# Performance work log

Hardware: AMD Instinct MI355X
Metric: run time of the kernel (lower is better)

The kernel has to match this reference:

```python
import jax, jax.numpy as jnp
import numpy as np

N_BONDS = 50000
N_EDGES = 600000
BOND_DIM = 64
SPH_DIM = 64
UNITS = 64


def setup_inputs() -> dict:
    key = jax.random.key(0)
    k1, k2, k3, k4, k5 = jax.random.split(key, 5)
    bond_features = jax.random.normal(k1, (N_BONDS, BOND_DIM), dtype=jnp.float32)
    edges_sph_features = jax.random.normal(k2, (N_EDGES, SPH_DIM), dtype=jnp.float32)
    # column 0: sorted segment ids (tf.math.segment_sum requires sorted ids)
    seg = jnp.sort(jax.random.randint(k3, (N_EDGES,), 0, N_BONDS, dtype=jnp.int32))
    nbr = jax.random.randint(k4, (N_EDGES,), 0, N_BONDS, dtype=jnp.int32)
    edges_neighbor = jnp.stack([seg, nbr], axis=1)  # [n_edges, 2]
    kernel = jax.random.normal(k5, (BOND_DIM + SPH_DIM, UNITS), dtype=jnp.float32) * 0.05
    bias = jnp.zeros((UNITS,), dtype=jnp.float32)
    return {
        "bond_features": bond_features,
        "edges_sph_features": edges_sph_features,
        "edges_neighbor": edges_neighbor,
        "kernel": kernel,
        "bias": bias,
    }


def reference(bond_features, edges_sph_features, edges_neighbor, kernel, bias):
    # gather bond features of the neighboring bond for each edge (line-graph)
    gathered = bond_features[edges_neighbor[:, 1]]            # [E, bond_dim]
    concated = jnp.concatenate([gathered, edges_sph_features], axis=-1)  # [E, bond_dim+sph_dim]
    # scatter-reduce into segments (sorted ids; fixed num_segments for jit)
    aggregated = jax.ops.segment_sum(
        concated, edges_neighbor[:, 0], num_segments=N_BONDS,
        indices_are_sorted=True,
    )  # [n_bonds, bond_dim+sph_dim]
    return aggregated @ kernel + bias
```

## Files before the change

### kernel.cpp

```cpp
#include <hip/hip_runtime.h>

#define N_BONDS 50000
#define N_EDGES 600000
#define R_BONDS 4
#define THREADS 512
#define BONDS_PER_BLOCK 32

typedef float f4 __attribute__((ext_vector_type(4)));

__device__ __forceinline__ float bcastf(float v, int l) {
    return __builtin_bit_cast(float, __builtin_amdgcn_readlane(__builtin_bit_cast(int, v), l));
}
__device__ __forceinline__ f4 f4zero() { return (f4){0.f, 0.f, 0.f, 0.f}; }
__device__ __forceinline__ void fma4(f4& a, float s, const f4& b) {
    a.x = fmaf(s, b.x, a.x); a.y = fmaf(s, b.y, a.y);
    a.z = fmaf(s, b.z, a.z); a.w = fmaf(s, b.w, a.w);
}

__global__ __launch_bounds__(256)
void fill_starts(const int* __restrict__ edges, int* __restrict__ starts) {
    const int e = blockIdx.x * blockDim.x + threadIdx.x;
    if (e >= N_EDGES) return;
    const int2* edges2 = (const int2*)edges;
    const int s  = edges2[e].x;
    const int sp = (e == 0) ? -1 : edges2[e - 1].x;
    for (int b = sp + 1; b <= s; ++b) starts[b] = e;
    if (e == N_EDGES - 1)
        for (int b = s + 1; b <= N_BONDS; ++b) starts[b] = N_EDGES;
}

__global__ __launch_bounds__(THREADS, 4)
void fused_gather_segsum_mm(const float* __restrict__ bond,
                            const float* __restrict__ sph,
                            const int*   __restrict__ edges,
                            const float* __restrict__ Kmat,
                            const float* __restrict__ bias,
                            const int*   __restrict__ starts,
                            float* __restrict__ out)
{
    __shared__ float ldsK[128 * 64];
    const int tid  = threadIdx.x;
    const int lane = tid & 63;
    const int wid  = tid >> 6;
    const int fl   = lane & 15;
    const int sg   = lane >> 4;

    {
        const f4* K4 = (const f4*)Kmat;
        f4*       L4 = (f4*)ldsK;
        #pragma unroll
        for (int i = 0; i < 4; ++i) L4[tid + i * THREADS] = K4[tid + i * THREADS];
    }
    __syncthreads();

    const int b0 = blockIdx.x * BONDS_PER_BLOCK + wid * R_BONDS;
    if (b0 >= N_BONDS) return;

    int st[R_BONDS + 1];
    #pragma unroll
    for (int r = 0; r <= R_BONDS; ++r)
        st[r] = __builtin_amdgcn_readfirstlane(starts[b0 + r]);

    const int eb    = st[0];
    const int total = st[R_BONDS] - eb;

    const f4*   bond4  = (const f4*)bond;
    const f4*   sph4   = (const f4*)sph;
    const int2* edges2 = (const int2*)edges;

    float slotG[R_BONDS], slotS[R_BONDS];
    f4 aG = f4zero(), aS = f4zero();
    int r = 0, cs = 0, bnd = st[1] - eb;

    auto txr = [&](f4 v) -> float {
        v.x += __shfl_xor(v.x, 16); v.y += __shfl_xor(v.y, 16);
        v.z += __shfl_xor(v.z, 16); v.w += __shfl_xor(v.w, 16);
        v.x += __shfl_xor(v.x, 32); v.y += __shfl_xor(v.y, 32);
        v.z += __shfl_xor(v.z, 32); v.w += __shfl_xor(v.w, 32);
        const int src = lane >> 2;
        const float s0 = __shfl(v.x, src), s1 = __shfl(v.y, src);
        const float s2 = __shfl(v.z, src), s3 = __shfl(v.w, src);
        const float r01 = (lane & 1) ? s1 : s0;
        const float r23 = (lane & 1) ? s3 : s2;
        return (lane & 2) ? r23 : r01;
    };

    auto slowpath = [&](int q, f4 GV, f4 SV) {
        const int qe = q + sg;
        while (true) {
            const float m = (qe >= cs && qe < bnd) ? 1.f : 0.f;
            fma4(aG, m, GV); fma4(aS, m, SV);
            if (bnd > q + 4) break;
            const float tG = txr(aG), tS = txr(aS);
            #pragma unroll
            for (int rr = 0; rr < R_BONDS; ++rr)
                if (rr == r) { slotG[rr] = tG; slotS[rr] = tS; }
            aG = f4zero(); aS = f4zero();
            cs = bnd;
            ++r;
            if (r >= R_BONDS) { bnd = 0x7fffffff; break; }
            #pragma unroll
            for (int rr = 2; rr <= R_BONDS; ++rr)
                if (r + 1 == rr) bnd = st[rr] - eb;
        }
    };

    int w0 = 0;
    while (w0 < total) {
        int wlen = total - w0; if (wlen > 64) wlen = 64;
        int2 p = make_int2(0, 0);
        if (lane < wlen) p = edges2[eb + w0 + lane];
        const int ng = (wlen + 3) >> 2;

        f4 gA, sA, gB, sB, gC, sC, gD, sD;

#define ISS(QQ, GV, SV) do { \
        if ((QQ) < ng) { \
            const int idx_ = (QQ) * 4 + sg; \
            const int nbr_ = __shfl(p.y, idx_); \
            int qe_ = w0 + idx_; if (qe_ >= total) qe_ = total - 1; \
            GV = bond4[nbr_ * 16 + fl]; \
            SV = __builtin_nontemporal_load(&sph4[(eb + qe_) * 16 + fl]); \
        } else { GV = f4zero(); SV = f4zero(); } } while (0)

#define ACC(QQ, GV, SV) do { \
        const int q_ = w0 + (QQ) * 4; \
        if (q_ + 4 <= bnd) { aG += GV; aS += SV; } \
        else slowpath(q_, GV, SV); } while (0)

        ISS(0, gA, sA); ISS(1, gB, sB); ISS(2, gC, sC); ISS(3, gD, sD);
        int q = 0;
        for (; q + 4 <= ng; q += 4) {
            ACC(q + 0, gA, sA); ISS(q + 4, gA, sA);
            ACC(q + 1, gB, sB); ISS(q + 5, gB, sB);
            ACC(q + 2, gC, sC); ISS(q + 6, gC, sC);
            ACC(q + 3, gD, sD); ISS(q + 7, gD, sD);
        }
        if (q + 0 < ng) ACC(q + 0, gA, sA);
        if (q + 1 < ng) ACC(q + 1, gB, sB);
        if (q + 2 < ng) ACC(q + 2, gC, sC);
#undef ISS
#undef ACC
        w0 += wlen;
    }

    {
        const float tG = txr(aG), tS = txr(aS);
        #pragma unroll
        for (int rr = 0; rr < R_BONDS; ++rr) {
            if (rr == r)     { slotG[rr] = tG;  slotS[rr] = tS; }
            else if (rr > r) { slotG[rr] = 0.f; slotS[rr] = 0.f; }
        }
    }

    float acc[R_BONDS];
    const float bl = bias[lane];
    #pragma unroll
    for (int rr = 0; rr < R_BONDS; ++rr) acc[rr] = bl;

    #pragma unroll 4
    for (int d = 0; d < 64; ++d) {
        const float kt = ldsK[d * 64 + lane];
        const float kb = ldsK[(64 + d) * 64 + lane];
        #pragma unroll
        for (int rr = 0; rr < R_BONDS; ++rr) {
            acc[rr] = fmaf(bcastf(slotG[rr], d), kt, acc[rr]);
            acc[rr] = fmaf(bcastf(slotS[rr], d), kb, acc[rr]);
        }
    }

    #pragma unroll
    for (int rr = 0; rr < R_BONDS; ++rr)
        if (b0 + rr < N_BONDS)
            __builtin_nontemporal_store(acc[rr], &out[(b0 + rr) * 64 + lane]);
}

extern "C" void kernel_launch(void* const* d_in, const int* in_sizes, int n_in,
                              void* d_out, int out_size, void* d_ws, size_t ws_size,
                              hipStream_t stream) {
    const float* bond  = (const float*)d_in[0];
    const float* sph   = (const float*)d_in[1];
    const int*   edges = (const int*)d_in[2];
    const float* Kmat  = (const float*)d_in[3];
    const float* bias  = (const float*)d_in[4];
    float* out  = (float*)d_out;
    int* starts = (int*)d_ws;

    fill_starts<<<(N_EDGES + 255) / 256, 256, 0, stream>>>(edges, starts);

    const int nblocks = (N_BONDS + BONDS_PER_BLOCK - 1) / BONDS_PER_BLOCK;
    fused_gather_segsum_mm<<<nblocks, THREADS, 0, stream>>>(bond, sph, edges, Kmat,
                                                            bias, starts, out);
}
```

Baseline: 76.43 us.

## Premultiply bond features by kernel before gather and split into three kernels

Uses linearity to multiply bond_features by the top half of the kernel once per bond, before the gather. The gather/segment-sum kernel then writes the reduced gathered part straight to out and the sph sum to a workspace buffer, and a final kernel applies the bottom half of the kernel plus bias. This removes the in-kernel matmul and the large LDS tile from the memory-bound gather loop, and it also moves to 8 bonds per wave with 256 threads. In exchange it adds two launches and extra round trips of 50000x64 intermediates through global memory. A fused fallback is kept for when the workspace is too small.

```diff
diff --git a/kernel.cpp b/kernel.cpp
--- a/kernel.cpp
+++ b/kernel.cpp
@@ -2,8 +2,8 @@
 
 #define N_BONDS 50000
 #define N_EDGES 600000
-#define R_BONDS 4
-#define THREADS 512
+#define R_BONDS 8
+#define THREADS 256
 #define BONDS_PER_BLOCK 32
 
 typedef float f4 __attribute__((ext_vector_type(4)));
@@ -29,49 +29,227 @@
         for (int b = s + 1; b <= N_BONDS; ++b) starts[b] = N_EDGES;
 }
 
+__global__ __launch_bounds__(256, 4)
+void premul_bond(const float* __restrict__ bond, const float* __restrict__ Kmat,
+                 float* __restrict__ bondK) {
+    __shared__ float ldsK[64 * 64];
+    const int tid = threadIdx.x, lane = tid & 63, wid = tid >> 6;
+    {
+        const f4* K4 = (const f4*)Kmat;
+        f4* L4 = (f4*)ldsK;
+        #pragma unroll
+        for (int i = 0; i < 4; ++i) L4[tid + i * 256] = K4[tid + i * 256];
+    }
+    __syncthreads();
+    const int row0 = blockIdx.x * BONDS_PER_BLOCK + wid * R_BONDS;
+    if (row0 >= N_BONDS) return;
+
+    float rowv[R_BONDS];
+    #pragma unroll
+    for (int r = 0; r < R_BONDS; ++r) {
+        int ri = row0 + r; if (ri >= N_BONDS) ri = N_BONDS - 1;
+        rowv[r] = __builtin_nontemporal_load(&bond[ri * 64 + lane]);
+    }
+    float acc[R_BONDS];
+    #pragma unroll
+    for (int r = 0; r < R_BONDS; ++r) acc[r] = 0.f;
+
+    #pragma unroll 4
+    for (int d = 0; d < 64; ++d) {
+        const float k = ldsK[d * 64 + lane];
+        #pragma unroll
+        for (int r = 0; r < R_BONDS; ++r)
+            acc[r] = fmaf(bcastf(rowv[r], d), k, acc[r]);
+    }
+    #pragma unroll
+    for (int r = 0; r < R_BONDS; ++r)
+        if (row0 + r < N_BONDS)
+            __builtin_nontemporal_store(acc[r], &bondK[(row0 + r) * 64 + lane]);
+}
+
 __global__ __launch_bounds__(THREADS, 4)
-void fused_gather_segsum_mm(const float* __restrict__ bond,
-                            const float* __restrict__ sph,
-                            const int*   __restrict__ edges,
-                            const float* __restrict__ Kmat,
-                            const float* __restrict__ bias,
-                            const int*   __restrict__ starts,
-                            float* __restrict__ out)
-{
-    __shared__ float ldsK[128 * 64];
-    const int tid  = threadIdx.x;
+void gather_segsum(const float* __restrict__ bondK, const float* __restrict__ sph,
+                   const int* __restrict__ edges, const int* __restrict__ starts,
+                   float* __restrict__ outG, float* __restrict__ Sbuf) {
+    const int tid = threadIdx.x;
     const int lane = tid & 63;
     const int wid  = tid >> 6;
     const int fl   = lane & 15;
     const int sg   = lane >> 4;
 
-    {
-        const f4* K4 = (const f4*)Kmat;
-        f4*       L4 = (f4*)ldsK;
-        #pragma unroll
-        for (int i = 0; i < 4; ++i) L4[tid + i * THREADS] = K4[tid + i * THREADS];
-    }
-    __syncthreads();
-
     const int b0 = blockIdx.x * BONDS_PER_BLOCK + wid * R_BONDS;
     if (b0 >= N_BONDS) return;
 
     int st[R_BONDS + 1];
     #pragma unroll
-    for (int r = 0; r <= R_BONDS; ++r)
-        st[r] = __builtin_amdgcn_readfirstlane(starts[b0 + r]);
-
-    const int eb    = st[0];
-    const int total = st[R_BONDS] - eb;
-
-    const f4*   bond4  = (const f4*)bond;
-    const f4*   sph4   = (const f4*)sph;
+    for (int r = 0; r <= R_BONDS; ++r) {
+        int ix = b0 + r; if (ix > N_BONDS) ix = N_BONDS;
+        st[r] = __builtin_amdgcn_readfirstlane(starts[ix]);
+    }
+    const int eb = st[0], total = st[R_BONDS] - eb;
+
+    const f4*   g4 = (const f4*)bondK;
+    const f4*   s4 = (const f4*)sph;
     const int2* edges2 = (const int2*)edges;
-
+    f4* oG = (f4*)outG;
+    f4* oS = (f4*)Sbuf;
+    const bool storer = (sg == 0);
+
+    f4 aG = f4zero(), aS = f4zero();
+    int r = 0, cs = 0, bnd = st[1] - eb;
+
+    auto xr = [&](f4 v) -> f4 {
+        v.x += __shfl_xor(v.x, 16); v.y += __shfl_xor(v.y, 16);
+        v.z += __shfl_xor(v.z, 16); v.w += __shfl_xor(v.w, 16);
+        v.x += __shfl_xor(v.x, 32); v.y += __shfl_xor(v.y, 32);
+        v.z += __shfl_xor(v.z, 32); v.w += __shfl_xor(v.w, 32);
+        return v;
+    };
+
+    auto slowpath = [&](int q, f4 GV, f4 SV) {
+        const int qe = q + sg;
+        while (true) {
+            const float m = (qe >= cs && qe < bnd) ? 1.f : 0.f;
+            fma4(aG, m, GV); fma4(aS, m, SV);
+            if (bnd > q + 4) break;
+            const f4 cg = xr(aG), csv = xr(aS);
+            if (storer && b0 + r < N_BONDS) {
+                __builtin_nontemporal_store(cg,  &oG[(b0 + r) * 16 + fl]);
+                __builtin_nontemporal_store(csv, &oS[(b0 + r) * 16 + fl]);
+            }
+            aG = f4zero(); aS = f4zero();
+            cs = bnd;
+            ++r;
+            if (r >= R_BONDS) { bnd = 0x7fffffff; break; }
+            #pragma unroll
+            for (int rr = 2; rr <= R_BONDS; ++rr)
+                if (r + 1 == rr) bnd = st[rr] - eb;
+        }
+    };
+
+    int w0 = 0;
+    while (w0 < total) {
+        int wlen = total - w0; if (wlen > 64) wlen = 64;
+        int2 p = make_int2(0, 0);
+        if (lane < wlen) p = edges2[eb + w0 + lane];
+        const int ng = (wlen + 3) >> 2;
+
+        f4 gA, sA, gB, sB, gC, sC, gD, sD;
+
+#define ISS(QQ, GV, SV) do { \
+        if ((QQ) < ng) { \
+            const int idx_ = (QQ) * 4 + sg; \
+            const int nbr_ = __shfl(p.y, idx_); \
+            int qe_ = w0 + idx_; if (qe_ >= total) qe_ = total - 1; \
+            GV = g4[nbr_ * 16 + fl]; \
+            SV = __builtin_nontemporal_load(&s4[(eb + qe_) * 16 + fl]); \
+        } else { GV = f4zero(); SV = f4zero(); } } while (0)
+
+#define ACC(QQ, GV, SV) do { \
+        const int q_ = w0 + (QQ) * 4; \
+        if (q_ + 4 <= bnd) { aG += GV; aS += SV; } \
+        else slowpath(q_, GV, SV); } while (0)
+
+        ISS(0, gA, sA); ISS(1, gB, sB); ISS(2, gC, sC); ISS(3, gD, sD);
+        int q = 0;
+        for (; q + 4 <= ng; q += 4) {
+            ACC(q + 0, gA, sA); ISS(q + 4, gA, sA);
+            ACC(q + 1, gB, sB); ISS(q + 5, gB, sB);
+            ACC(q + 2, gC, sC); ISS(q + 6, gC, sC);
+            ACC(q + 3, gD, sD); ISS(q + 7, gD, sD);
+        }
+        if (q + 0 < ng) ACC(q + 0, gA, sA);
+        if (q + 1 < ng) ACC(q + 1, gB, sB);
+        if (q + 2 < ng) ACC(q + 2, gC, sC);
+#undef ISS
+#undef ACC
+        w0 += wlen;
+    }
+
+    {
+        const f4 cg = xr(aG), csv = xr(aS);
+        if (r < R_BONDS && storer && b0 + r < N_BONDS) {
+            __builtin_nontemporal_store(cg,  &oG[(b0 + r) * 16 + fl]);
+            __builtin_nontemporal_store(csv, &oS[(b0 + r) * 16 + fl]);
+        }
+        const f4 z = f4zero();
+        for (int bb = r + 1; bb < R_BONDS; ++bb) {
+            if (storer && b0 + bb < N_BONDS) {
+                __builtin_nontemporal_store(z, &oG[(b0 + bb) * 16 + fl]);
+                __builtin_nontemporal_store(z, &oS[(b0 + bb) * 16 + fl]);
+            }
+        }
+    }
+}
+
+__global__ __launch_bounds__(256, 4)
+void finish_mm(const float* __restrict__ Sbuf, const float* __restrict__ Kmat,
+               const float* __restrict__ bias, float* __restrict__ out) {
+    __shared__ float ldsK[64 * 64];
+    const int tid = threadIdx.x, lane = tid & 63, wid = tid >> 6;
+    {
+        const f4* K4 = (const f4*)Kmat;
+        f4* L4 = (f4*)ldsK;
+        #pragma unroll
+        for (int i = 0; i < 4; ++i) L4[tid + i * 256] = K4[1024 + tid + i * 256];
+    }
+    __syncthreads();
+    const int row0 = blockIdx.x * BONDS_PER_BLOCK + wid * R_BONDS;
+    if (row0 >= N_BONDS) return;
+
+    const float bl = bias[lane];
+    float rowv[R_BONDS], acc[R_BONDS];
+    #pragma unroll
+    for (int r = 0; r < R_BONDS; ++r) {
+        int ri = row0 + r; if (ri >= N_BONDS) ri = N_BONDS - 1;
+        rowv[r] = __builtin_nontemporal_load(&Sbuf[ri * 64 + lane]);
+        acc[r]  = out[ri * 64 + lane] + bl;
+    }
+    #pragma unroll 4
+    for (int d = 0; d < 64; ++d) {
+        const float k = ldsK[d * 64 + lane];
+        #pragma unroll
+        for (int r = 0; r < R_BONDS; ++r)
+            acc[r] = fmaf(bcastf(rowv[r], d), k, acc[r]);
+    }
+    #pragma unroll
+    for (int r = 0; r < R_BONDS; ++r)
+        if (row0 + r < N_BONDS)
+            __builtin_nontemporal_store(acc[r], &out[(row0 + r) * 64 + lane]);
+}
+
+__global__ __launch_bounds__(THREADS, 4)
+void fused_fallback(const float* __restrict__ bond, const float* __restrict__ sph,
+                    const int* __restrict__ edges, const float* __restrict__ Kmat,
+                    const float* __restrict__ bias, const int* __restrict__ starts,
+                    float* __restrict__ out) {
+    __shared__ float ldsK[128 * 64];
+    const int tid = threadIdx.x, lane = tid & 63, wid = tid >> 6;
+    const int fl = lane & 15, sg = lane >> 4;
+    const float bl = bias[lane];
+    const int b0 = blockIdx.x * BONDS_PER_BLOCK + wid * R_BONDS;
+    int stv[R_BONDS + 1];
+    #pragma unroll
+    for (int r = 0; r <= R_BONDS; ++r) {
+        int ix = b0 + r; if (ix > N_BONDS) ix = N_BONDS;
+        stv[r] = starts[ix];
+    }
+    {
+        const f4* K4 = (const f4*)Kmat; f4* L4 = (f4*)ldsK;
+        #pragma unroll
+        for (int i = 0; i < 8; ++i) L4[tid + i * THREADS] = K4[tid + i * THREADS];
+    }
+    __syncthreads();
+    if (b0 >= N_BONDS) return;
+    int st[R_BONDS + 1];
+    #pragma unroll
+    for (int r = 0; r <= R_BONDS; ++r) st[r] = __builtin_amdgcn_readfirstlane(stv[r]);
+    const int eb = st[0], total = st[R_BONDS] - eb;
+    const f4* bond4 = (const f4*)bond; const f4* sph4 = (const f4*)sph;
+    const int2* edges2 = (const int2*)edges;
     float slotG[R_BONDS], slotS[R_BONDS];
     f4 aG = f4zero(), aS = f4zero();
     int r = 0, cs = 0, bnd = st[1] - eb;
-
     auto txr = [&](f4 v) -> float {
         v.x += __shfl_xor(v.x, 16); v.y += __shfl_xor(v.y, 16);
         v.z += __shfl_xor(v.z, 16); v.w += __shfl_xor(v.w, 16);
@@ -84,7 +262,6 @@
         const float r23 = (lane & 1) ? s3 : s2;
         return (lane & 2) ? r23 : r01;
     };
-
     auto slowpath = [&](int q, f4 GV, f4 SV) {
         const int qe = q + sg;
         while (true) {
@@ -96,24 +273,20 @@
             for (int rr = 0; rr < R_BONDS; ++rr)
                 if (rr == r) { slotG[rr] = tG; slotS[rr] = tS; }
             aG = f4zero(); aS = f4zero();
-            cs = bnd;
-            ++r;
+            cs = bnd; ++r;
             if (r >= R_BONDS) { bnd = 0x7fffffff; break; }
             #pragma unroll
             for (int rr = 2; rr <= R_BONDS; ++rr)
                 if (r + 1 == rr) bnd = st[rr] - eb;
         }
     };
-
     int w0 = 0;
     while (w0 < total) {
         int wlen = total - w0; if (wlen > 64) wlen = 64;
         int2 p = make_int2(0, 0);
         if (lane < wlen) p = edges2[eb + w0 + lane];
         const int ng = (wlen + 3) >> 2;
-
         f4 gA, sA, gB, sB, gC, sC, gD, sD;
-
 #define ISS(QQ, GV, SV) do { \
         if ((QQ) < ng) { \
             const int idx_ = (QQ) * 4 + sg; \
@@ -122,12 +295,10 @@
             GV = bond4[nbr_ * 16 + fl]; \
             SV = __builtin_nontemporal_load(&sph4[(eb + qe_) * 16 + fl]); \
         } else { GV = f4zero(); SV = f4zero(); } } while (0)
-
 #define ACC(QQ, GV, SV) do { \
         const int q_ = w0 + (QQ) * 4; \
         if (q_ + 4 <= bnd) { aG += GV; aS += SV; } \
         else slowpath(q_, GV, SV); } while (0)
-
         ISS(0, gA, sA); ISS(1, gB, sB); ISS(2, gC, sC); ISS(3, gD, sD);
         int q = 0;
         for (; q + 4 <= ng; q += 4) {
@@ -143,7 +314,6 @@
 #undef ACC
         w0 += wlen;
     }
-
     {
         const float tG = txr(aG), tS = txr(aS);
         #pragma unroll
@@ -152,12 +322,9 @@
             else if (rr > r) { slotG[rr] = 0.f; slotS[rr] = 0.f; }
         }
     }
-
     float acc[R_BONDS];
-    const float bl = bias[lane];
     #pragma unroll
     for (int rr = 0; rr < R_BONDS; ++rr) acc[rr] = bl;
-
     #pragma unroll 4
     for (int d = 0; d < 64; ++d) {
         const float kt = ldsK[d * 64 + lane];
@@ -168,7 +335,6 @@
             acc[rr] = fmaf(bcastf(slotS[rr], d), kb, acc[rr]);
         }
     }
-
     #pragma unroll
     for (int rr = 0; rr < R_BONDS; ++rr)
         if (b0 + rr < N_BONDS)
@@ -183,12 +349,24 @@
     const int*   edges = (const int*)d_in[2];
     const float* Kmat  = (const float*)d_in[3];
     const float* bias  = (const float*)d_in[4];
-    float* out  = (float*)d_out;
-    int* starts = (int*)d_ws;
+    float* out = (float*)d_out;
+
+    int*   starts = (int*)d_ws;
+    float* bondK  = (float*)((char*)d_ws + 262144);
+    float* Sbuf   = (float*)((char*)d_ws + 262144 + (size_t)N_BONDS * 64 * 4);
+
+    const size_t need = 262144 + 2ull * N_BONDS * 64 * 4;
+    const int nblocks = (N_BONDS + BONDS_PER_BLOCK - 1) / BONDS_PER_BLOCK;
 
     fill_starts<<<(N_EDGES + 255) / 256, 256, 0, stream>>>(edges, starts);
 
-    const int nblocks = (N_BONDS + BONDS_PER_BLOCK - 1) / BONDS_PER_BLOCK;
-    fused_gather_segsum_mm<<<nblocks, THREADS, 0, stream>>>(bond, sph, edges, Kmat,
-                                                            bias, starts, out);
-}
+    if (ws_size >= need) {
+        premul_bond<<<nblocks, 256, 0, stream>>>(bond, Kmat, bondK);
+        gather_segsum<<<nblocks, THREADS, 0, stream>>>(bondK, sph, edges, starts,
+                                                       out, Sbuf);
+        finish_mm<<<nblocks, 256, 0, stream>>>(Sbuf, Kmat, bias, out);
+    } else {
+        fused_fallback<<<nblocks, THREADS, 0, stream>>>(bond, sph, edges, Kmat,
+                                                        bias, starts, out);
+    }
+}
```

Measured after the change: 104.3 us. 36.5% more time.
